# Optimization experiments

Hardware: AMD Instinct MI355X
Metric: run time of the kernel (lower is better)

The kernel has to match this reference:

```python
import jax, jax.numpy as jnp
import numpy as np

DIM = 1024
HEADS = 16
HEAD_DIM = DIM // HEADS
B, N = 2, 2048


def setup_inputs() -> dict:
    key = jax.random.key(0)
    k1, k2, k3, k4 = jax.random.split(key, 4)
    x = jax.random.normal(k1, (B, N, DIM), dtype=jnp.float32)
    # torch Linear weights: shape (out_features, in_features), y = x @ W.T + b
    w_qkv = jax.random.normal(k2, (3 * DIM, DIM), dtype=jnp.float32) * (DIM ** -0.5)
    w_proj = jax.random.normal(k3, (DIM, DIM), dtype=jnp.float32) * (DIM ** -0.5)
    b_proj = jax.random.normal(k4, (DIM,), dtype=jnp.float32) * 0.01
    return {"x": x, "w_qkv": w_qkv, "w_proj": w_proj, "b_proj": b_proj}


def reference(x, w_qkv, w_proj, b_proj):
    Bb, Nn, D = x.shape
    scale = HEAD_DIM ** -0.5
    qkv = x @ w_qkv.T                                # [B, N, 3D]
    qkv = qkv.reshape(Bb, Nn, 3, HEADS, HEAD_DIM)
    qkv = jnp.transpose(qkv, (2, 0, 3, 1, 4))        # [3, B, H, N, hd]
    q, k, v = qkv[0], qkv[1], qkv[2]
    attn = jnp.einsum('bhqd,bhkd->bhqk', q, k) * scale
    attn = jax.nn.softmax(attn, axis=-1)
    out = jnp.einsum('bhqk,bhkd->bhqd', attn, v)     # [B, H, N, hd]
    out = jnp.transpose(out, (0, 2, 1, 3)).reshape(Bb, Nn, D)
    return out @ w_proj.T + b_proj
```

## Files before the change

kernel.cpp:

```cpp
#include <hip/hip_runtime.h>
#include <hip/hip_bf16.h>
#include <cstdint>
#include <cstddef>

using u16 = unsigned short;
using u32 = uint32_t;
using f32x4  = __attribute__((ext_vector_type(4))) float;
using bf16x8 = __attribute__((ext_vector_type(8))) __bf16;
using s16x4  = __attribute__((ext_vector_type(4))) short;

#define D_MODEL 1024
#define N_HEADS 16
#define HD      64
#define SEQ     2048
#define QKV_LD  3072
#define K2SCALE 0.18033688011112042f

__device__ __forceinline__ u16 f2b(float f) {
  union { float f; u32 u; } v; v.f = f;
  u32 r = 0x7FFFu + ((v.u >> 16) & 1u);
  return (u16)((v.u + r) >> 16);
}

__device__ __forceinline__ u32 pkbf16(float a, float b) {
  union { __hip_bfloat162 h; u32 u; } c;
  c.h = __float22bfloat162_rn(float2{a, b});
  return c.u;
}

#define MFMA16(A, B, C) __builtin_amdgcn_mfma_f32_16x16x16bf16_1k(A, B, C, 0, 0, 0)

__device__ __forceinline__ void gld16(const u16* g, u16* l) {
  __builtin_amdgcn_global_load_lds(
      (const __attribute__((address_space(1))) void*)g,
      (__attribute__((address_space(3))) void*)l, 16, 0, 0);
}

__global__ void cast3_bf16(const float* __restrict__ x, const float* __restrict__ wq,
                           const float* __restrict__ wp, u16* __restrict__ dst) {
  int i = blockIdx.x * blockDim.x + threadIdx.x;
  const float* src;
  int off;
  if (blockIdx.x < 4096)      { src = x;  off = 0; }
  else if (blockIdx.x < 7168) { src = wq; off = 4096 * 256; }
  else                        { src = wp; off = 7168 * 256; }
  float4 f = ((const float4*)src)[i - off];
  u32 lo = pkbf16(f.x, f.y), hi = pkbf16(f.z, f.w);
  uint2 o = {lo, hi};
  ((uint2*)dst)[i] = o;
}

template<int OUTMODE, int MT>
__launch_bounds__(256, 3)
__global__ void gemm_nt(const u16* __restrict__ A, const u16* __restrict__ B,
                        u16* __restrict__ Ob, float* __restrict__ Of,
                        const float* __restrict__ bias, int N, int K) {
  __shared__ __attribute__((aligned(16))) u16 sA[2][MT * 32];
  __shared__ __attribute__((aligned(16))) u16 sB[2][128 * 32];

  const int tid  = threadIdx.x;
  const int lane = tid & 63;
  const int w    = tid >> 6;
  const int qd   = lane >> 4;
  const int ln   = lane & 15;
  constexpr int MI = MT / 32;
  const int wm   = (w >> 1) * (MT / 2);
  const int wn   = (w & 1) * 64;

  const int nbx = gridDim.x;
  const int lin = blockIdx.y * nbx + blockIdx.x;
  const int cpx = (nbx * gridDim.y) >> 3;
  const int swz = (lin & 7) * cpx + (lin >> 3);
  const int m0  = (swz / nbx) * MT;
  const int n0  = (swz % nbx) * 128;

  auto stage = [&](int kk, int buf) {
    int k0 = kk * 32;
    #pragma unroll
    for (int c = 0; c < MT / 64; ++c) {
      int sbase = w * MT + c * 64;
      int s = sbase + lane;
      int line = s >> 3, sub = (s & 7) ^ (line & 7);
      int row = line * 2 + (sub >> 2), col = (sub & 3) * 8;
      gld16(A + (size_t)(m0 + row) * K + k0 + col, &sA[buf][sbase * 8]);
    }
    #pragma unroll
    for (int c = 0; c < 2; ++c) {
      int sbase = w * 128 + c * 64;
      int s = sbase + lane;
      int line = s >> 3, sub = (s & 7) ^ (line & 7);
      int row = line * 2 + (sub >> 2), col = (sub & 3) * 8;
      gld16(B + (size_t)(n0 + row) * K + k0 + col, &sB[buf][sbase * 8]);
    }
  };

  f32x4 acc[MI][4] = {};
  const int NK = K >> 5;
  stage(0, 0);

  for (int kk = 0; kk < NK; ++kk) {
    const int cur = kk & 1;
    __syncthreads();
    if (kk + 1 < NK) stage(kk + 1, cur ^ 1);

    bf16x8 af[MI], bfm[4];
    #pragma unroll
    for (int i = 0; i < MI; ++i) {
      int r = wm + i * 16 + ln;
      af[i] = *(const bf16x8*)&sA[cur][(r >> 1) * 64 +
                ((((r & 1) << 5) + qd * 8) ^ (((r >> 1) & 7) << 3))];
    }
    #pragma unroll
    for (int j = 0; j < 4; ++j) {
      int r = wn + j * 16 + ln;
      bfm[j] = *(const bf16x8*)&sB[cur][(r >> 1) * 64 +
                ((((r & 1) << 5) + qd * 8) ^ (((r >> 1) & 7) << 3))];
    }
    #pragma unroll
    for (int i = 0; i < MI; ++i)
      #pragma unroll
      for (int j = 0; j < 4; ++j)
        acc[i][j] = __builtin_amdgcn_mfma_f32_16x16x32_bf16(af[i], bfm[j], acc[i][j], 0, 0, 0);
  }

  #pragma unroll
  for (int i = 0; i < MI; ++i) {
    #pragma unroll
    for (int j = 0; j < 4; ++j) {
      #pragma unroll
      for (int r = 0; r < 4; ++r) {
        int row = m0 + wm + i * 16 + qd * 4 + r;
        int col = n0 + wn + j * 16 + ln;
        float v = acc[i][j][r];
        if (OUTMODE == 0) {
          if (col < D_MODEL) v *= K2SCALE;
          Ob[(size_t)row * N + col] = f2b(v);
        } else {
          Of[(size_t)row * N + col] = v + bias[col];
        }
      }
    }
  }
}

__launch_bounds__(256, 2)
__global__ void attn_kernel(const u16* __restrict__ qkv, u16* __restrict__ outb) {
  __shared__ __attribute__((aligned(16))) u16 smem[20480];
  u16 (*sK)[64 * 64] = (u16(*)[64 * 64])smem;
  u32* const sVT0 = (u32*)(smem + 8192);
  u32* const sVT1 = sVT0 + 64 * 32;
  u32* const sVT2 = sVT1 + 64 * 32;

  const int tid  = threadIdx.x;
  const int lane = tid & 63;
  const int w    = tid >> 6;
  const int qd   = lane >> 4;
  const int ln   = lane & 15;
  const int qp   = blockIdx.x;
  const int h    = blockIdx.y & 15;
  const int b    = blockIdx.y >> 4;
  const size_t tokbase = (size_t)b * SEQ;
  const int q0   = qp * 128;
  const int qoff = h * HD;
  const int koff = D_MODEL + h * HD;
  const int voff = 2 * D_MODEL + h * HD;

  bf16x8 aq[2][2];
  #pragma unroll
  for (int c2 = 0; c2 < 2; ++c2)
    #pragma unroll
    for (int hf = 0; hf < 2; ++hf)
      aq[c2][hf] = *(const bf16x8*)(qkv + (tokbase + q0 + c2 * 64 + w * 16 + ln) * QKV_LD
                                    + qoff + hf * 32 + qd * 8);

  auto stageK = [&](int kt, int buf) {
    #pragma unroll
    for (int c = 0; c < 2; ++c) {
      int sbase = c * 256 + w * 64;
      int s = sbase + lane;
      int row = s >> 3, sub = (s & 7) ^ (row & 7);
      gld16(qkv + (tokbase + kt * 64 + row) * QKV_LD + koff + sub * 8,
            &sK[buf][sbase * 8]);
    }
  };
  auto loadV = [&](int kt, uint4& va, uint4& vb) {
    int tp = tid & 31, d0 = (tid >> 5) * 8;
    const u16* g0 = qkv + (tokbase + kt * 64 + tp * 2) * QKV_LD + voff + d0;
    va = *(const uint4*)g0;
    vb = *(const uint4*)(g0 + QKV_LD);
  };
  auto writeV = [&](u32* vbuf, const uint4& va, const uint4& vb) {
    int tp = tid & 31, d0 = (tid >> 5) * 8;
    const u32* a  = (const u32*)&va;
    const u32* bb = (const u32*)&vb;
    #pragma unroll
    for (int e = 0; e < 4; ++e) {
      vbuf[(d0 + 2 * e    ) * 32 + (tp ^ (e << 3)    )] =
          __builtin_amdgcn_perm(bb[e], a[e], 0x05040100u);
      vbuf[(d0 + 2 * e + 1) * 32 + (tp ^ (e << 3) ^ 4)] =
          __builtin_amdgcn_perm(bb[e], a[e], 0x07060302u);
    }
  };

  f32x4 accOT[2][4] = {};
  f32x4 stA[4][2], stB[4][2];
  float psum[2] = {0.f, 0.f};
  const int tsw = (ln & 7) << 2;
  const int ksw = (ln & 7) << 3;

  auto qk_phase = [&](int t, f32x4 (&stW)[4][2]) {
    const int cur = t & 1;
    #pragma unroll
    for (int cb = 0; cb < 4; ++cb) {
      bf16x8 ak0 = *(const bf16x8*)&sK[cur][(cb * 16 + ln) * 64 + ((qd * 8) ^ ksw)];
      bf16x8 ak1 = *(const bf16x8*)&sK[cur][(cb * 16 + ln) * 64 + ((32 + qd * 8) ^ ksw)];
      #pragma unroll
      for (int c2 = 0; c2 < 2; ++c2) {
        f32x4 z = {0.f, 0.f, 0.f, 0.f};
        f32x4 t0 = __builtin_amdgcn_mfma_f32_16x16x32_bf16(ak0, aq[c2][0], z, 0, 0, 0);
        stW[cb][c2] = __builtin_amdgcn_mfma_f32_16x16x32_bf16(ak1, aq[c2][1], t0, 0, 0, 0);
      }
    }
  };
  auto fin_phase = [&](f32x4 (&stR)[4][2], const u32* vP) {
    #pragma unroll
    for (int cb = 0; cb < 4; ++cb) {
      s16x4 pf[2];
      #pragma unroll
      for (int c2 = 0; c2 < 2; ++c2) {
        float p0 = __builtin_amdgcn_exp2f(stR[cb][c2][0]);
        float p1 = __builtin_amdgcn_exp2f(stR[cb][c2][1]);
        float p2 = __builtin_amdgcn_exp2f(stR[cb][c2][2]);
        float p3 = __builtin_amdgcn_exp2f(stR[cb][c2][3]);
        psum[c2] += (p0 + p1) + (p2 + p3);
        union { u32 d[2]; s16x4 v; } pk;
        pk.d[0] = pkbf16(p0, p1);
        pk.d[1] = pkbf16(p2, p3);
        pf[c2] = pk.v;
      }
      #pragma unroll
      for (int ob = 0; ob < 4; ++ob) {
        s16x4 vf = *(const s16x4*)&vP[(ob * 16 + ln) * 32 + ((cb * 8 + qd * 2) ^ tsw)];
        accOT[0][ob] = MFMA16(vf, pf[0], accOT[0][ob]);
        accOT[1][ob] = MFMA16(vf, pf[1], accOT[1][ob]);
      }
    }
  };

  stageK(0, 0);
  uint4 va, vb;
  loadV(0, va, vb);
  writeV(sVT0, va, vb);
  loadV(1, va, vb);
  u32 *vPrev = sVT2, *vCur = sVT0, *vNext = sVT1;

  __syncthreads();
  stageK(1, 1);
  writeV(vNext, va, vb);
  loadV(2, va, vb);
  qk_phase(0, stA);
  { u32* t = vPrev; vPrev = vCur; vCur = vNext; vNext = t; }

  for (int S = 0; S < 15; ++S) {
    const int t1 = 2 * S + 1;
    __syncthreads();
    stageK(t1 + 1, (t1 + 1) & 1);
    writeV(vNext, va, vb);
    loadV(t1 + 2, va, vb);
    qk_phase(t1, stB);
    fin_phase(stA, vPrev);
    { u32* t = vPrev; vPrev = vCur; vCur = vNext; vNext = t; }
    const int t2 = t1 + 1;
    __syncthreads();
    stageK(t2 + 1, (t2 + 1) & 1);
    writeV(vNext, va, vb);
    if (t2 < 30) loadV(t2 + 2, va, vb);
    qk_phase(t2, stA);
    fin_phase(stB, vPrev);
    { u32* t = vPrev; vPrev = vCur; vCur = vNext; vNext = t; }
  }

  __syncthreads();
  qk_phase(31, stB);
  fin_phase(stA, vPrev);
  fin_phase(stB, vCur);

  #pragma unroll
  for (int c2 = 0; c2 < 2; ++c2) {
    float s = psum[c2];
    s += __shfl_xor(s, 16, 64);
    s += __shfl_xor(s, 32, 64);
    psum[c2] = 1.0f / s;
  }

  u16* sOut = smem;
  __syncthreads();
  #pragma unroll
  for (int c2 = 0; c2 < 2; ++c2)
    #pragma unroll
    for (int ob = 0; ob < 4; ++ob) {
      u32 lo = pkbf16(accOT[c2][ob][0] * psum[c2], accOT[c2][ob][1] * psum[c2]);
      u32 hi = pkbf16(accOT[c2][ob][2] * psum[c2], accOT[c2][ob][3] * psum[c2]);
      ((u32*)sOut)[(c2 * 64 + w * 16 + ln) * 36 + ob * 8 + qd * 2    ] = lo;
      ((u32*)sOut)[(c2 * 64 + w * 16 + ln) * 36 + ob * 8 + qd * 2 + 1] = hi;
    }
  __syncthreads();
  #pragma unroll
  for (int it = 0; it < 4; ++it) {
    int idx = it * 256 + tid;
    int token = idx >> 3, chunk = idx & 7;
    uint4 v = *(const uint4*)&sOut[token * 72 + chunk * 8];
    *(uint4*)&outb[(tokbase + q0 + token) * D_MODEL + h * HD + chunk * 8] = v;
  }
}

extern "C" void kernel_launch(void* const* d_in, const int* in_sizes, int n_in,
                              void* d_out, int out_size, void* d_ws, size_t ws_size,
                              hipStream_t stream) {
  const float* x      = (const float*)d_in[0];
  const float* w_qkv  = (const float*)d_in[1];
  const float* w_proj = (const float*)d_in[2];
  const float* b_proj = (const float*)d_in[3];
  float* out = (float*)d_out;

  u16* ws     = (u16*)d_ws;
  u16* xb     = ws;
  u16* wqkvb  = xb    + (size_t)4096 * 1024;
  u16* wprojb = wqkvb + (size_t)3072 * 1024;
  u16* qkvb   = wprojb + (size_t)1024 * 1024;
  u16* attnb  = qkvb  + (size_t)4096 * 3072;

  cast3_bf16<<<8192, 256, 0, stream>>>(x, w_qkv, w_proj, xb);

  gemm_nt<0, 128><<<dim3(24, 32), 256, 0, stream>>>(xb, wqkvb, qkvb, nullptr, nullptr, 3072, 1024);

  attn_kernel<<<dim3(16, 32), 256, 0, stream>>>(qkvb, attnb);

  gemm_nt<1, 64><<<dim3(8, 64), 256, 0, stream>>>(attnb, wprojb, nullptr, out, b_proj, 1024, 1024);
}
```

Baseline: 182.6 us.

## Use dedicated 256x256-tile, 512-thread GEMM for the QKV projection

Replaces the 128x128-tile QKV GEMM with a dedicated kernel that uses 256x256 output tiles, 8 waves, K-step 64 with XOR-swizzled LDS and direct global-to-LDS loads. Next-stage loads are interleaved with the MFMA phases, and s_setprio raises priority during the MFMA bursts. The larger tile raises arithmetic intensity and LDS reuse, but the grid shrinks to 192 blocks on a 256-CU part, so occupancy and load balance may suffer. The projection GEMM is simplified to a float-output-only template.

```diff
diff --git a/kernel.cpp b/kernel.cpp
--- a/kernel.cpp
+++ b/kernel.cpp
@@ -50,10 +50,116 @@
   ((uint2*)dst)[i] = o;
 }
 
-template<int OUTMODE, int MT>
+__launch_bounds__(512, 2)
+__global__ void gemm_qkv_256(const u16* __restrict__ A, const u16* __restrict__ B,
+                             u16* __restrict__ Ob, int N, int K) {
+  __shared__ __attribute__((aligned(16))) u16 sA[2][256 * 64];
+  __shared__ __attribute__((aligned(16))) u16 sB[2][256 * 64];
+
+  const int tid  = threadIdx.x;
+  const int lane = tid & 63;
+  const int w    = tid >> 6;
+  const int qd   = lane >> 4;
+  const int ln   = lane & 15;
+  const int wm   = (w >> 2) * 128;
+  const int wn   = (w & 3) * 64;
+
+  const int nbx = gridDim.x;
+  const int lin = blockIdx.y * nbx + blockIdx.x;
+  const int cpx = (nbx * gridDim.y) >> 3;
+  const int swz = (lin & 7) * cpx + (lin >> 3);
+  const int m0  = (swz / nbx) * 256;
+  const int n0  = (swz % nbx) * 256;
+
+  auto stage_half = [&](int kt, int buf, int p) {
+    u16* dst = (p < 2) ? sA[buf] : sB[buf];
+    const u16* src = (p < 2) ? (A + (size_t)m0 * K) : (B + (size_t)n0 * K);
+    const int hb = (p & 1) * 1024;
+    #pragma unroll
+    for (int is = 0; is < 2; ++is) {
+      int s = hb + is * 512 + tid;
+      int row = s >> 3, ch = (s & 7) ^ (row & 7);
+      gld16(src + (size_t)row * K + kt * 64 + ch * 8, dst + s * 8);
+    }
+  };
+  auto rdA = [&](int buf, int r, int s8) {
+    return *(const bf16x8*)&sA[buf][r * 64 + (((s8 * 4 + qd) ^ (r & 7)) << 3)];
+  };
+  auto rdB = [&](int buf, int r, int s8) {
+    return *(const bf16x8*)&sB[buf][r * 64 + (((s8 * 4 + qd) ^ (r & 7)) << 3)];
+  };
+
+  #pragma unroll
+  for (int p = 0; p < 4; ++p) stage_half(0, 0, p);
+
+  f32x4 acc[8][4] = {};
+  const int NT = K >> 6;
+
+  for (int j = 0; j < NT; ++j) {
+    const int cb = j & 1, nb = cb ^ 1;
+    if (j + 1 < NT) {
+      stage_half(j + 1, nb, 0);
+      asm volatile("s_waitcnt vmcnt(2)" ::: "memory");
+    } else {
+      asm volatile("s_waitcnt vmcnt(0)" ::: "memory");
+    }
+    __builtin_amdgcn_s_barrier();
+    asm volatile("" ::: "memory");
+
+    #pragma unroll
+    for (int mh = 0; mh < 2; ++mh) {
+      bf16x8 af[4][2];
+      #pragma unroll
+      for (int mi = 0; mi < 4; ++mi) {
+        int r = wm + (mh * 4 + mi) * 16 + ln;
+        af[mi][0] = rdA(cb, r, 0);
+        af[mi][1] = rdA(cb, r, 1);
+      }
+      #pragma unroll
+      for (int nh = 0; nh < 2; ++nh) {
+        const int ph = mh * 2 + nh;
+        if (ph > 0 && j + 1 < NT) stage_half(j + 1, nb, ph);
+        bf16x8 bfr[2][2];
+        #pragma unroll
+        for (int nj = 0; nj < 2; ++nj) {
+          int r = wn + (nh * 2 + nj) * 16 + ln;
+          bfr[nj][0] = rdB(cb, r, 0);
+          bfr[nj][1] = rdB(cb, r, 1);
+        }
+        __builtin_amdgcn_s_setprio(1);
+        #pragma unroll
+        for (int mi = 0; mi < 4; ++mi)
+          #pragma unroll
+          for (int nj = 0; nj < 2; ++nj) {
+            f32x4 c = acc[mh * 4 + mi][nh * 2 + nj];
+            c = __builtin_amdgcn_mfma_f32_16x16x32_bf16(af[mi][0], bfr[nj][0], c, 0, 0, 0);
+            c = __builtin_amdgcn_mfma_f32_16x16x32_bf16(af[mi][1], bfr[nj][1], c, 0, 0, 0);
+            acc[mh * 4 + mi][nh * 2 + nj] = c;
+          }
+        __builtin_amdgcn_s_setprio(0);
+      }
+    }
+    asm volatile("" ::: "memory");
+    __builtin_amdgcn_s_barrier();
+  }
+
+  const float scl = (n0 < D_MODEL) ? K2SCALE : 1.0f;
+  #pragma unroll
+  for (int mf = 0; mf < 8; ++mf)
+    #pragma unroll
+    for (int nf = 0; nf < 4; ++nf)
+      #pragma unroll
+      for (int r = 0; r < 4; ++r) {
+        int row = m0 + wm + mf * 16 + qd * 4 + r;
+        int col = n0 + wn + nf * 16 + ln;
+        Ob[(size_t)row * N + col] = f2b(acc[mf][nf][r] * scl);
+      }
+}
+
+template<int MT>
 __launch_bounds__(256, 3)
 __global__ void gemm_nt(const u16* __restrict__ A, const u16* __restrict__ B,
-                        u16* __restrict__ Ob, float* __restrict__ Of,
+                        float* __restrict__ Of,
                         const float* __restrict__ bias, int N, int K) {
   __shared__ __attribute__((aligned(16))) u16 sA[2][MT * 32];
   __shared__ __attribute__((aligned(16))) u16 sB[2][128 * 32];
@@ -124,23 +230,15 @@
   }
 
   #pragma unroll
-  for (int i = 0; i < MI; ++i) {
-    #pragma unroll
-    for (int j = 0; j < 4; ++j) {
+  for (int i = 0; i < MI; ++i)
+    #pragma unroll
+    for (int j = 0; j < 4; ++j)
       #pragma unroll
       for (int r = 0; r < 4; ++r) {
         int row = m0 + wm + i * 16 + qd * 4 + r;
         int col = n0 + wn + j * 16 + ln;
-        float v = acc[i][j][r];
-        if (OUTMODE == 0) {
-          if (col < D_MODEL) v *= K2SCALE;
-          Ob[(size_t)row * N + col] = f2b(v);
-        } else {
-          Of[(size_t)row * N + col] = v + bias[col];
-        }
-      }
-    }
-  }
+        Of[(size_t)row * N + col] = acc[i][j][r] + bias[col];
+      }
 }
 
 __launch_bounds__(256, 2)
@@ -332,9 +430,9 @@
 
   cast3_bf16<<<8192, 256, 0, stream>>>(x, w_qkv, w_proj, xb);
 
-  gemm_nt<0, 128><<<dim3(24, 32), 256, 0, stream>>>(xb, wqkvb, qkvb, nullptr, nullptr, 3072, 1024);
+  gemm_qkv_256<<<dim3(12, 16), 512, 0, stream>>>(xb, wqkvb, qkvb, 3072, 1024);
 
   attn_kernel<<<dim3(16, 32), 256, 0, stream>>>(qkvb, attnb);
 
-  gemm_nt<1, 64><<<dim3(8, 64), 256, 0, stream>>>(attnb, wprojb, nullptr, out, b_proj, 1024, 1024);
-}
+  gemm_nt<64><<<dim3(8, 64), 256, 0, stream>>>(attnb, wprojb, out, b_proj, 1024, 1024);
+}
```

After: 185.5 us. Within noise of the previous version (+1.6%).
